# Kernel optimization log

Measured on AMD Instinct MI355X. Metric: run time of the kernel, lower is better.

## Reference

```python
import jax, jax.numpy as jnp
import numpy as np

N_HEADS = 16
D_EMBD = 1024
T = 4096


def setup_inputs() -> dict:
    key = jax.random.key(0)
    k0, k1, k2 = jax.random.split(key, 3)
    scale1 = 1.0 / np.sqrt(D_EMBD)
    x = jax.random.normal(k0, (T, D_EMBD), dtype=jnp.float32)
    W1 = jax.random.normal(k1, (D_EMBD, 3 * D_EMBD), dtype=jnp.float32) * scale1
    b1 = jnp.zeros((3 * D_EMBD,), dtype=jnp.float32)
    W2 = jax.random.normal(k2, (D_EMBD, D_EMBD), dtype=jnp.float32) * scale1
    b2 = jnp.zeros((D_EMBD,), dtype=jnp.float32)
    return {"x": x, "W1": W1, "b1": b1, "W2": W2, "b2": b2}


def reference(x, W1, b1, W2, b2):
    T_, D = x.shape
    d_head = D // N_HEADS
    kqv = x @ W1 + b1                       # (T, 3D)
    k, q, v = jnp.split(kqv, 3, axis=-1)    # note original order: k, q, v
    # t (h d) -> h t d
    def to_heads(t):
        return t.reshape(T_, N_HEADS, d_head).transpose(1, 0, 2)
    q, k, v = to_heads(q), to_heads(k), to_heads(v)
    # causal masked retention: mask * (q k^T) @ v, no softmax
    scores = jnp.einsum('htd,hsd->hts', q, k)          # (H, T, T)
    mask = jnp.tril(jnp.ones((T_, T_), dtype=bool))
    scores = jnp.where(mask, scores, 0.0)
    out = jnp.einsum('hts,hsd->htd', scores, v)        # (H, T, d)
    out = out.transpose(1, 0, 2).reshape(T_, D)        # h t d -> t (h d)
    return out @ W2 + b2
```

## Files before the change

kernel.cpp:

```cpp
#include <hip/hip_runtime.h>
#include <hip/hip_bf16.h>

#define TSEQ 4096
#define DE   1024
#define NH   16
#define DH   64
#define LD3  3072
#define NCH  64

typedef float4 f4;
typedef unsigned short u16;
typedef __attribute__((ext_vector_type(8))) short s16x8;
typedef __attribute__((ext_vector_type(4))) float f32x4;

__device__ inline u16 f2bf(float f) {
    unsigned int u = __float_as_uint(f);
    u += 0x7FFF + ((u >> 16) & 1);
    return (u16)(u >> 16);
}

__global__ __launch_bounds__(256) void cast_f32_bf16(const float* __restrict__ in,
                                                     u16* __restrict__ out, int n4) {
    int i = blockIdx.x * 256 + threadIdx.x;
    if (i < n4) {
        f4 v = *reinterpret_cast<const f4*>(&in[(size_t)i * 4]);
        ushort4 o = make_ushort4(f2bf(v.x), f2bf(v.y), f2bf(v.z), f2bf(v.w));
        *reinterpret_cast<ushort4*>(&out[(size_t)i * 4]) = o;
    }
}

__global__ __launch_bounds__(256) void transpose_cast_f32(
    const float* __restrict__ in, u16* __restrict__ out,
    int in_ld, int out_ld) {
    __shared__ u16 Ts[64][65];
    const int tid = threadIdx.x;
    const int r0 = blockIdx.y * 64, c0 = blockIdx.x * 64;
    #pragma unroll
    for (int l = 0; l < 4; ++l) {
        int f = tid + 256 * l, r = f >> 4, c = (f & 15) * 4;
        f4 v = *reinterpret_cast<const f4*>(&in[(size_t)(r0 + r) * in_ld + c0 + c]);
        Ts[c + 0][r] = f2bf(v.x); Ts[c + 1][r] = f2bf(v.y);
        Ts[c + 2][r] = f2bf(v.z); Ts[c + 3][r] = f2bf(v.w);
    }
    __syncthreads();
    #pragma unroll
    for (int l = 0; l < 2; ++l) {
        int f = tid + 256 * l, r2 = f >> 3, c2 = (f & 7) * 8;
        union { u16 u[8]; f4 v; } pk;
        #pragma unroll
        for (int j = 0; j < 8; ++j) pk.u[j] = Ts[r2][c2 + j];
        *reinterpret_cast<f4*>(&out[(size_t)(c0 + r2) * out_ld + r0 + c2]) = pk.v;
    }
}

__global__ __launch_bounds__(256) void transpose_bf16(
    const u16* __restrict__ in, u16* __restrict__ out,
    int in_ld, int out_ld) {
    __shared__ u16 Ts[64][65];
    const int tid = threadIdx.x;
    const int r0 = blockIdx.y * 64, c0 = blockIdx.x * 64;
    #pragma unroll
    for (int l = 0; l < 2; ++l) {
        int f = tid + 256 * l, r = f >> 3, c = (f & 7) * 8;
        union { u16 u[8]; f4 v; } pk;
        pk.v = *reinterpret_cast<const f4*>(&in[(size_t)(r0 + r) * in_ld + c0 + c]);
        #pragma unroll
        for (int j = 0; j < 8; ++j) Ts[c + j][r] = pk.u[j];
    }
    __syncthreads();
    #pragma unroll
    for (int l = 0; l < 2; ++l) {
        int f = tid + 256 * l, r2 = f >> 3, c2 = (f & 7) * 8;
        union { u16 u[8]; f4 v; } pk;
        #pragma unroll
        for (int j = 0; j < 8; ++j) pk.u[j] = Ts[r2][c2 + j];
        *reinterpret_cast<f4*>(&out[(size_t)(c0 + r2) * out_ld + r0 + c2]) = pk.v;
    }
}

__device__ inline void gl_lds16(const void* g, void* l) {
    __builtin_amdgcn_global_load_lds(
        (const __attribute__((address_space(1))) void*)g,
        (__attribute__((address_space(3))) void*)l, 16, 0, 0);
}

template<bool OUT_BF16>
__global__ __launch_bounds__(256) void gemm_mfma(
    const u16* __restrict__ A, const u16* __restrict__ Bt,
    const float* __restrict__ bias, void* __restrict__ Cout,
    int M, int N, int K) {
    __shared__ u16 As[128][32];
    __shared__ u16 Bs[128][32];
    const int tid = threadIdx.x;
    const int m0 = blockIdx.y * 128, n0 = blockIdx.x * 128;
    const int w = tid >> 6, lid = tid & 63, ln = tid & 15, quad = (tid & 63) >> 4;
    const int wm = (w >> 1) * 64, wn = (w & 1) * 64;
    const int srow = lid >> 2, scol = (lid & 3) * 8;

    f32x4 acc[4][4];
    #pragma unroll
    for (int i = 0; i < 4; ++i)
        #pragma unroll
        for (int j = 0; j < 4; ++j) acc[i][j] = 0.f;

    for (int k0 = 0; k0 < K; k0 += 32) {
        __syncthreads();
        #pragma unroll
        for (int i = 0; i < 2; ++i) {
            const int rb = w * 16 + i * 64;
            gl_lds16(&A[(size_t)(m0 + rb + srow) * K + k0 + scol], &As[rb][0]);
            gl_lds16(&Bt[(size_t)(n0 + rb + srow) * K + k0 + scol], &Bs[rb][0]);
        }
        __syncthreads();
        s16x8 a[4], b[4];
        #pragma unroll
        for (int mt = 0; mt < 4; ++mt)
            a[mt] = *reinterpret_cast<const s16x8*>(&As[wm + mt * 16 + ln][quad * 8]);
        #pragma unroll
        for (int nt = 0; nt < 4; ++nt)
            b[nt] = *reinterpret_cast<const s16x8*>(&Bs[wn + nt * 16 + ln][quad * 8]);
        #pragma unroll
        for (int mt = 0; mt < 4; ++mt)
            #pragma unroll
            for (int nt = 0; nt < 4; ++nt)
                acc[mt][nt] = __builtin_amdgcn_mfma_f32_16x16x32_bf16(
                    a[mt], b[nt], acc[mt][nt], 0, 0, 0);
    }

    float bv[4];
    #pragma unroll
    for (int nt = 0; nt < 4; ++nt) bv[nt] = bias[n0 + wn + nt * 16 + ln];
    #pragma unroll
    for (int mt = 0; mt < 4; ++mt)
        #pragma unroll
        for (int nt = 0; nt < 4; ++nt)
            #pragma unroll
            for (int r = 0; r < 4; ++r) {
                int row = m0 + wm + mt * 16 + quad * 4 + r;
                int col = n0 + wn + nt * 16 + ln;
                float v = acc[mt][nt][r] + bv[nt];
                if (OUT_BF16) ((u16*)Cout)[(size_t)row * N + col] = f2bf(v);
                else          ((float*)Cout)[(size_t)row * N + col] = v;
            }
}

__global__ __launch_bounds__(256) void gchunk_kernel(
    const u16* __restrict__ Ktg, const u16* __restrict__ Vtg,
    float* __restrict__ Gt) {
    const int tid = threadIdx.x;
    const int w = tid >> 6, ln = tid & 15, quad = (tid & 63) >> 4;
    const int gw = blockIdx.x * 4 + w;
    const int h = gw & 15, c = gw >> 4;

    s16x8 kf[4][2], vf[4][2];
    #pragma unroll
    for (int mt = 0; mt < 4; ++mt)
        #pragma unroll
        for (int kk = 0; kk < 2; ++kk)
            kf[mt][kk] = *reinterpret_cast<const s16x8*>(
                &Ktg[(size_t)(h * DH + mt * 16 + ln) * TSEQ + c * 64 + kk * 32 + quad * 8]);
    #pragma unroll
    for (int nt = 0; nt < 4; ++nt)
        #pragma unroll
        for (int kk = 0; kk < 2; ++kk)
            vf[nt][kk] = *reinterpret_cast<const s16x8*>(
                &Vtg[(size_t)(h * DH + nt * 16 + ln) * TSEQ + c * 64 + kk * 32 + quad * 8]);

    f32x4 acc[4][4];
    #pragma unroll
    for (int i = 0; i < 4; ++i)
        #pragma unroll
        for (int j = 0; j < 4; ++j) acc[i][j] = 0.f;
    #pragma unroll
    for (int mt = 0; mt < 4; ++mt)
        #pragma unroll
        for (int nt = 0; nt < 4; ++nt)
            #pragma unroll
            for (int kk = 0; kk < 2; ++kk)
                acc[mt][nt] = __builtin_amdgcn_mfma_f32_16x16x32_bf16(
                    kf[mt][kk], vf[nt][kk], acc[mt][nt], 0, 0, 0);

    float* base = &Gt[((size_t)(c * 16 + h) << 12)];
    #pragma unroll
    for (int mt = 0; mt < 4; ++mt)
        #pragma unroll
        for (int nt = 0; nt < 4; ++nt)
            *reinterpret_cast<f4*>(
                &base[(nt * 16 + ln) * 64 + mt * 16 + quad * 4]) =
                make_float4(acc[mt][nt][0], acc[mt][nt][1],
                            acc[mt][nt][2], acc[mt][nt][3]);
}

__global__ __launch_bounds__(256) void prefix_scan(
    const float* __restrict__ Gt, u16* __restrict__ P) {
    const int t = blockIdx.x * 256 + threadIdx.x;
    const int h = t >> 12, e = t & 4095;
    float sum = 0.f;
    for (int c = 0; c < NCH; ++c) {
        size_t a = ((size_t)(c * 16 + h) << 12) + e;
        P[a] = f2bf(sum);
        sum += Gt[a];
    }
}

__global__ __launch_bounds__(256, 2) void intra_mfma(
    const u16* __restrict__ kqvb, const u16* __restrict__ Vtg,
    const u16* __restrict__ P, u16* __restrict__ attnb) {
    __shared__ u16 Ss[4][16][72];
    const int tid = threadIdx.x;
    const int w = tid >> 6, ln = tid & 15, quad = (tid & 63) >> 4;
    const int qt = blockIdx.x, h = blockIdx.y;
    const int q0 = qt * 64;

    s16x8 qf[2];
    #pragma unroll
    for (int kk = 0; kk < 2; ++kk)
        qf[kk] = *reinterpret_cast<const s16x8*>(
            &kqvb[(size_t)(q0 + w * 16 + ln) * LD3 + DE + h * DH + kk * 32 + quad * 8]);

    s16x8 kf[4][2];
    #pragma unroll
    for (int mt = 0; mt < 4; ++mt)
        #pragma unroll
        for (int kk = 0; kk < 2; ++kk)
            kf[mt][kk] = *reinterpret_cast<const s16x8*>(
                &kqvb[(size_t)(q0 + mt * 16 + ln) * LD3 + h * DH + kk * 32 + quad * 8]);

    #pragma unroll
    for (int mt = 0; mt < 4; ++mt) {
        f32x4 s;
        s = 0.f;
        s = __builtin_amdgcn_mfma_f32_16x16x32_bf16(kf[mt][0], qf[0], s, 0, 0, 0);
        s = __builtin_amdgcn_mfma_f32_16x16x32_bf16(kf[mt][1], qf[1], s, 0, 0, 0);
        #pragma unroll
        for (int r = 0; r < 4; ++r)
            if (mt * 16 + quad * 4 + r > w * 16 + ln) s[r] = 0.f;
        __hip_bfloat162 p0 = __float22bfloat162_rn(make_float2(s[0], s[1]));
        __hip_bfloat162 p1 = __float22bfloat162_rn(make_float2(s[2], s[3]));
        uint2 pk = make_uint2(*reinterpret_cast<unsigned int*>(&p0),
                              *reinterpret_cast<unsigned int*>(&p1));
        *reinterpret_cast<uint2*>(&Ss[w][ln][mt * 16 + quad * 4]) = pk;
    }

    s16x8 sf[2];
    #pragma unroll
    for (int kk = 0; kk < 2; ++kk)
        sf[kk] = *reinterpret_cast<const s16x8*>(&Ss[w][ln][kk * 32 + quad * 8]);

    f32x4 accO[4];
    #pragma unroll
    for (int nt = 0; nt < 4; ++nt) accO[nt] = 0.f;

    #pragma unroll
    for (int nt = 0; nt < 4; ++nt)
        #pragma unroll
        for (int kk = 0; kk < 2; ++kk) {
            s16x8 vf = *reinterpret_cast<const s16x8*>(
                &Vtg[(size_t)(h * DH + nt * 16 + ln) * TSEQ + q0 + kk * 32 + quad * 8]);
            accO[nt] = __builtin_amdgcn_mfma_f32_16x16x32_bf16(sf[kk], vf, accO[nt], 0, 0, 0);
        }

    const u16* Pc = P + (((size_t)(qt * 16 + h)) << 12);
    #pragma unroll
    for (int nt = 0; nt < 4; ++nt)
        #pragma unroll
        for (int kk = 0; kk < 2; ++kk) {
            s16x8 pf = *reinterpret_cast<const s16x8*>(
                &Pc[(nt * 16 + ln) * 64 + kk * 32 + quad * 8]);
            accO[nt] = __builtin_amdgcn_mfma_f32_16x16x32_bf16(qf[kk], pf, accO[nt], 0, 0, 0);
        }

    #pragma unroll
    for (int nt = 0; nt < 4; ++nt)
        #pragma unroll
        for (int r = 0; r < 4; ++r)
            attnb[(size_t)(q0 + w * 16 + quad * 4 + r) * DE + h * DH + nt * 16 + ln] =
                f2bf(accO[nt][r]);
}

extern "C" void kernel_launch(void* const* d_in, const int* in_sizes, int n_in,
                              void* d_out, int out_size, void* d_ws, size_t ws_size,
                              hipStream_t stream) {
    const float* x  = (const float*)d_in[0];
    const float* W1 = (const float*)d_in[1];
    const float* b1 = (const float*)d_in[2];
    const float* W2 = (const float*)d_in[3];
    const float* b2 = (const float*)d_in[4];
    float* out = (float*)d_out;

    u16* xb    = (u16*)d_ws;
    u16* W1t   = xb    + (size_t)TSEQ * DE;
    u16* W2t   = W1t   + (size_t)LD3 * DE;
    u16* kqvb  = W2t   + (size_t)DE * DE;
    u16* Ktg   = kqvb  + (size_t)TSEQ * LD3;
    u16* Vtg   = Ktg   + (size_t)DE * TSEQ;
    float* Gt  = (float*)(Vtg + (size_t)DE * TSEQ);
    u16* P     = xb;
    u16* attnb = (u16*)Gt;

    cast_f32_bf16<<<(TSEQ * DE / 4 + 255) / 256, 256, 0, stream>>>(x, xb, TSEQ * DE / 4);
    transpose_cast_f32<<<dim3(LD3 / 64, DE / 64), 256, 0, stream>>>(W1, W1t, LD3, DE);
    transpose_cast_f32<<<dim3(DE / 64, DE / 64), 256, 0, stream>>>(W2, W2t, DE, DE);

    gemm_mfma<true><<<dim3(LD3 / 128, TSEQ / 128), 256, 0, stream>>>(
        xb, W1t, b1, kqvb, TSEQ, LD3, DE);

    transpose_bf16<<<dim3(DE / 64, TSEQ / 64), 256, 0, stream>>>(kqvb, Ktg, LD3, TSEQ);
    transpose_bf16<<<dim3(DE / 64, TSEQ / 64), 256, 0, stream>>>(
        kqvb + 2 * DE, Vtg, LD3, TSEQ);

    gchunk_kernel<<<NCH * NH / 4, 256, 0, stream>>>(Ktg, Vtg, Gt);
    prefix_scan<<<NH * 4096 / 256, 256, 0, stream>>>(Gt, P);
    intra_mfma<<<dim3(NCH, NH), 256, 0, stream>>>(kqvb, Vtg, P, attnb);

    gemm_mfma<false><<<dim3(DE / 128, TSEQ / 128), 256, 0, stream>>>(
        attnb, W2t, b2, out, TSEQ, DE, DE);
}
```

Baseline: 189.2 us.

## Fuse prep casts into one kernel and transpose K/V in LDS inside consumers

The three cast/transpose launches for x, W1 and W2 are merged into a single prep kernel that dispatches on block index. The two global K/V transpose kernels and their workspace buffers are removed. gchunk_kernel and intra_mfma now load K and V tiles straight from the QKV GEMM output and transpose them through LDS. This cuts kernel launches and a full write and reread of transposed K/V, at the cost of LDS transposes with strided shared-memory writes. The prefix scan also software-pipelines its global load.

After: 176.5 us. -6.7%, faster.

```diff
diff --git a/kernel.cpp b/kernel.cpp
--- a/kernel.cpp
+++ b/kernel.cpp
@@ -19,22 +19,36 @@
     return (u16)(u >> 16);
 }
 
-__global__ __launch_bounds__(256) void cast_f32_bf16(const float* __restrict__ in,
-                                                     u16* __restrict__ out, int n4) {
-    int i = blockIdx.x * 256 + threadIdx.x;
-    if (i < n4) {
-        f4 v = *reinterpret_cast<const f4*>(&in[(size_t)i * 4]);
+__device__ inline void gl_lds16(const void* g, void* l) {
+    __builtin_amdgcn_global_load_lds(
+        (const __attribute__((address_space(1))) void*)g,
+        (__attribute__((address_space(3))) void*)l, 16, 0, 0);
+}
+
+__global__ __launch_bounds__(256) void prep_kernel(
+    const float* __restrict__ x, const float* __restrict__ W1,
+    const float* __restrict__ W2, u16* __restrict__ xb,
+    u16* __restrict__ W1t, u16* __restrict__ W2t) {
+    __shared__ u16 Ts[64][65];
+    const int b = blockIdx.x, tid = threadIdx.x;
+
+    if (b < 4096) {
+        int i = b * 256 + tid;
+        f4 v = *reinterpret_cast<const f4*>(&x[(size_t)i * 4]);
         ushort4 o = make_ushort4(f2bf(v.x), f2bf(v.y), f2bf(v.z), f2bf(v.w));
-        *reinterpret_cast<ushort4*>(&out[(size_t)i * 4]) = o;
-    }
-}
-
-__global__ __launch_bounds__(256) void transpose_cast_f32(
-    const float* __restrict__ in, u16* __restrict__ out,
-    int in_ld, int out_ld) {
-    __shared__ u16 Ts[64][65];
-    const int tid = threadIdx.x;
-    const int r0 = blockIdx.y * 64, c0 = blockIdx.x * 64;
+        *reinterpret_cast<ushort4*>(&xb[(size_t)i * 4]) = o;
+        return;
+    }
+    const float* in; u16* out; int in_ld, out_ld, r0, c0;
+    if (b < 4864) {
+        int i = b - 4096;
+        in = W1; out = W1t; in_ld = LD3; out_ld = DE;
+        r0 = (i / 48) * 64; c0 = (i % 48) * 64;
+    } else {
+        int i = b - 4864;
+        in = W2; out = W2t; in_ld = DE; out_ld = DE;
+        r0 = (i / 16) * 64; c0 = (i % 16) * 64;
+    }
     #pragma unroll
     for (int l = 0; l < 4; ++l) {
         int f = tid + 256 * l, r = f >> 4, c = (f & 15) * 4;
@@ -51,37 +65,6 @@
         for (int j = 0; j < 8; ++j) pk.u[j] = Ts[r2][c2 + j];
         *reinterpret_cast<f4*>(&out[(size_t)(c0 + r2) * out_ld + r0 + c2]) = pk.v;
     }
-}
-
-__global__ __launch_bounds__(256) void transpose_bf16(
-    const u16* __restrict__ in, u16* __restrict__ out,
-    int in_ld, int out_ld) {
-    __shared__ u16 Ts[64][65];
-    const int tid = threadIdx.x;
-    const int r0 = blockIdx.y * 64, c0 = blockIdx.x * 64;
-    #pragma unroll
-    for (int l = 0; l < 2; ++l) {
-        int f = tid + 256 * l, r = f >> 3, c = (f & 7) * 8;
-        union { u16 u[8]; f4 v; } pk;
-        pk.v = *reinterpret_cast<const f4*>(&in[(size_t)(r0 + r) * in_ld + c0 + c]);
-        #pragma unroll
-        for (int j = 0; j < 8; ++j) Ts[c + j][r] = pk.u[j];
-    }
-    __syncthreads();
-    #pragma unroll
-    for (int l = 0; l < 2; ++l) {
-        int f = tid + 256 * l, r2 = f >> 3, c2 = (f & 7) * 8;
-        union { u16 u[8]; f4 v; } pk;
-        #pragma unroll
-        for (int j = 0; j < 8; ++j) pk.u[j] = Ts[r2][c2 + j];
-        *reinterpret_cast<f4*>(&out[(size_t)(c0 + r2) * out_ld + r0 + c2]) = pk.v;
-    }
-}
-
-__device__ inline void gl_lds16(const void* g, void* l) {
-    __builtin_amdgcn_global_load_lds(
-        (const __attribute__((address_space(1))) void*)g,
-        (__attribute__((address_space(3))) void*)l, 16, 0, 0);
 }
 
 template<bool OUT_BF16>
@@ -144,74 +127,88 @@
             }
 }
 
-__global__ __launch_bounds__(256) void gchunk_kernel(
-    const u16* __restrict__ Ktg, const u16* __restrict__ Vtg,
-    float* __restrict__ Gt) {
+__global__ __launch_bounds__(256, 2) void gchunk_kernel(
+    const u16* __restrict__ kqvb, float* __restrict__ Gt) {
+    __shared__ u16 KT[64][72];
+    __shared__ u16 VT[64][72];
     const int tid = threadIdx.x;
     const int w = tid >> 6, ln = tid & 15, quad = (tid & 63) >> 4;
-    const int gw = blockIdx.x * 4 + w;
-    const int h = gw & 15, c = gw >> 4;
-
-    s16x8 kf[4][2], vf[4][2];
-    #pragma unroll
-    for (int mt = 0; mt < 4; ++mt)
-        #pragma unroll
-        for (int kk = 0; kk < 2; ++kk)
-            kf[mt][kk] = *reinterpret_cast<const s16x8*>(
-                &Ktg[(size_t)(h * DH + mt * 16 + ln) * TSEQ + c * 64 + kk * 32 + quad * 8]);
-    #pragma unroll
-    for (int nt = 0; nt < 4; ++nt)
-        #pragma unroll
-        for (int kk = 0; kk < 2; ++kk)
-            vf[nt][kk] = *reinterpret_cast<const s16x8*>(
-                &Vtg[(size_t)(h * DH + nt * 16 + ln) * TSEQ + c * 64 + kk * 32 + quad * 8]);
-
-    f32x4 acc[4][4];
-    #pragma unroll
-    for (int i = 0; i < 4; ++i)
-        #pragma unroll
-        for (int j = 0; j < 4; ++j) acc[i][j] = 0.f;
-    #pragma unroll
-    for (int mt = 0; mt < 4; ++mt)
-        #pragma unroll
-        for (int nt = 0; nt < 4; ++nt)
-            #pragma unroll
-            for (int kk = 0; kk < 2; ++kk)
-                acc[mt][nt] = __builtin_amdgcn_mfma_f32_16x16x32_bf16(
-                    kf[mt][kk], vf[nt][kk], acc[mt][nt], 0, 0, 0);
+    const int c = blockIdx.x, h = blockIdx.y;
+
+    #pragma unroll
+    for (int l = 0; l < 2; ++l) {
+        int idx = tid + 256 * l, t = idx >> 3, dc = (idx & 7) * 8;
+        const size_t rb = (size_t)(c * 64 + t) * LD3 + h * DH + dc;
+        union { u16 u[8]; f4 v; } pk;
+        pk.v = *reinterpret_cast<const f4*>(&kqvb[rb]);
+        #pragma unroll
+        for (int j = 0; j < 8; ++j) KT[dc + j][t] = pk.u[j];
+        pk.v = *reinterpret_cast<const f4*>(&kqvb[rb + 2 * DE]);
+        #pragma unroll
+        for (int j = 0; j < 8; ++j) VT[dc + j][t] = pk.u[j];
+    }
+    __syncthreads();
+
+    s16x8 kf[2];
+    #pragma unroll
+    for (int kk = 0; kk < 2; ++kk)
+        kf[kk] = *reinterpret_cast<const s16x8*>(&KT[w * 16 + ln][kk * 32 + quad * 8]);
+
+    f32x4 acc[4];
+    #pragma unroll
+    for (int nt = 0; nt < 4; ++nt) acc[nt] = 0.f;
+    #pragma unroll
+    for (int nt = 0; nt < 4; ++nt)
+        #pragma unroll
+        for (int kk = 0; kk < 2; ++kk) {
+            s16x8 vf = *reinterpret_cast<const s16x8*>(&VT[nt * 16 + ln][kk * 32 + quad * 8]);
+            acc[nt] = __builtin_amdgcn_mfma_f32_16x16x32_bf16(kf[kk], vf, acc[nt], 0, 0, 0);
+        }
 
     float* base = &Gt[((size_t)(c * 16 + h) << 12)];
     #pragma unroll
-    for (int mt = 0; mt < 4; ++mt)
-        #pragma unroll
-        for (int nt = 0; nt < 4; ++nt)
-            *reinterpret_cast<f4*>(
-                &base[(nt * 16 + ln) * 64 + mt * 16 + quad * 4]) =
-                make_float4(acc[mt][nt][0], acc[mt][nt][1],
-                            acc[mt][nt][2], acc[mt][nt][3]);
+    for (int nt = 0; nt < 4; ++nt)
+        *reinterpret_cast<f4*>(&base[(nt * 16 + ln) * 64 + w * 16 + quad * 4]) =
+            make_float4(acc[nt][0], acc[nt][1], acc[nt][2], acc[nt][3]);
 }
 
 __global__ __launch_bounds__(256) void prefix_scan(
     const float* __restrict__ Gt, u16* __restrict__ P) {
     const int t = blockIdx.x * 256 + threadIdx.x;
     const int h = t >> 12, e = t & 4095;
+    const size_t stride = (size_t)16 << 12;
+    size_t a = ((size_t)h << 12) + e;
     float sum = 0.f;
+    float nxt = Gt[a];
     for (int c = 0; c < NCH; ++c) {
-        size_t a = ((size_t)(c * 16 + h) << 12) + e;
+        float cur = nxt;
+        if (c + 1 < NCH) nxt = Gt[a + stride];
         P[a] = f2bf(sum);
-        sum += Gt[a];
+        sum += cur;
+        a += stride;
     }
 }
 
 __global__ __launch_bounds__(256, 2) void intra_mfma(
-    const u16* __restrict__ kqvb, const u16* __restrict__ Vtg,
-    const u16* __restrict__ P, u16* __restrict__ attnb) {
+    const u16* __restrict__ kqvb, const u16* __restrict__ P,
+    u16* __restrict__ attnb) {
+    __shared__ u16 VT[64][72];
     __shared__ u16 Ss[4][16][72];
     const int tid = threadIdx.x;
     const int w = tid >> 6, ln = tid & 15, quad = (tid & 63) >> 4;
     const int qt = blockIdx.x, h = blockIdx.y;
     const int q0 = qt * 64;
 
+    #pragma unroll
+    for (int l = 0; l < 2; ++l) {
+        int idx = tid + 256 * l, t = idx >> 3, dc = (idx & 7) * 8;
+        union { u16 u[8]; f4 v; } pk;
+        pk.v = *reinterpret_cast<const f4*>(
+            &kqvb[(size_t)(q0 + t) * LD3 + 2 * DE + h * DH + dc]);
+        #pragma unroll
+        for (int j = 0; j < 8; ++j) VT[dc + j][t] = pk.u[j];
+    }
+
     s16x8 qf[2];
     #pragma unroll
     for (int kk = 0; kk < 2; ++kk)
@@ -225,6 +222,8 @@
         for (int kk = 0; kk < 2; ++kk)
             kf[mt][kk] = *reinterpret_cast<const s16x8*>(
                 &kqvb[(size_t)(q0 + mt * 16 + ln) * LD3 + h * DH + kk * 32 + quad * 8]);
+
+    __syncthreads();
 
     #pragma unroll
     for (int mt = 0; mt < 4; ++mt) {
@@ -255,8 +254,7 @@
     for (int nt = 0; nt < 4; ++nt)
         #pragma unroll
         for (int kk = 0; kk < 2; ++kk) {
-            s16x8 vf = *reinterpret_cast<const s16x8*>(
-                &Vtg[(size_t)(h * DH + nt * 16 + ln) * TSEQ + q0 + kk * 32 + quad * 8]);
+            s16x8 vf = *reinterpret_cast<const s16x8*>(&VT[nt * 16 + ln][kk * 32 + quad * 8]);
             accO[nt] = __builtin_amdgcn_mfma_f32_16x16x32_bf16(sf[kk], vf, accO[nt], 0, 0, 0);
         }
 
@@ -292,26 +290,18 @@
     u16* W1t   = xb    + (size_t)TSEQ * DE;
     u16* W2t   = W1t   + (size_t)LD3 * DE;
     u16* kqvb  = W2t   + (size_t)DE * DE;
-    u16* Ktg   = kqvb  + (size_t)TSEQ * LD3;
-    u16* Vtg   = Ktg   + (size_t)DE * TSEQ;
-    float* Gt  = (float*)(Vtg + (size_t)DE * TSEQ);
+    float* Gt  = (float*)(kqvb + (size_t)TSEQ * LD3);
     u16* P     = xb;
     u16* attnb = (u16*)Gt;
 
-    cast_f32_bf16<<<(TSEQ * DE / 4 + 255) / 256, 256, 0, stream>>>(x, xb, TSEQ * DE / 4);
-    transpose_cast_f32<<<dim3(LD3 / 64, DE / 64), 256, 0, stream>>>(W1, W1t, LD3, DE);
-    transpose_cast_f32<<<dim3(DE / 64, DE / 64), 256, 0, stream>>>(W2, W2t, DE, DE);
+    prep_kernel<<<5120, 256, 0, stream>>>(x, W1, W2, xb, W1t, W2t);
 
     gemm_mfma<true><<<dim3(LD3 / 128, TSEQ / 128), 256, 0, stream>>>(
         xb, W1t, b1, kqvb, TSEQ, LD3, DE);
 
-    transpose_bf16<<<dim3(DE / 64, TSEQ / 64), 256, 0, stream>>>(kqvb, Ktg, LD3, TSEQ);
-    transpose_bf16<<<dim3(DE / 64, TSEQ / 64), 256, 0, stream>>>(
-        kqvb + 2 * DE, Vtg, LD3, TSEQ);
-
-    gchunk_kernel<<<NCH * NH / 4, 256, 0, stream>>>(Ktg, Vtg, Gt);
+    gchunk_kernel<<<dim3(NCH, NH), 256, 0, stream>>>(kqvb, Gt);
     prefix_scan<<<NH * 4096 / 256, 256, 0, stream>>>(Gt, P);
-    intra_mfma<<<dim3(NCH, NH), 256, 0, stream>>>(kqvb, Vtg, P, attnb);
+    intra_mfma<<<dim3(NCH, NH), 256, 0, stream>>>(kqvb, P, attnb);
 
     gemm_mfma<false><<<dim3(DE / 128, TSEQ / 128), 256, 0, stream>>>(
         attnb, W2t, b2, out, TSEQ, DE, DE);
```
